# Kernel optimization log

Measured on AMD Instinct MI355X. Metric: run time of the kernel, lower is better.

Reference implementation:

```python
import jax, jax.numpy as jnp
import numpy as np

NUM_MID = 10   # hard-coded num_mid_nodes in HiPool.__init__
NUM_HIGH = 5   # ceil(10 / 2)


def map_low_to_high(num_low, num_high):
    # eye(num_high) repeat_interleaved by ceil(low/high) rows, truncated to num_low
    # == one-hot of i // edges_per_high
    edges_per_high = -(-num_low // num_high)
    return jax.nn.one_hot(jnp.arange(num_low) // edges_per_high, num_high,
                          dtype=jnp.float32)  # [low, high]


def cluster_attention(x, mapping, att):
    # x: [s, d], mapping: [s, m], att: [d, d]
    mid = mapping.T @ x                              # [m, d]
    scores = (mid @ att) @ x.T                       # [m, s]
    scores = scores * (1.0 - mapping).T              # zero (not -inf) own-cluster entries, as in source
    scores = jax.nn.softmax(scores, axis=1)
    return scores @ x + mid                          # [m, d]


def dense_gcn(x, adj, W, b):
    # torch_geometric DenseGCNConv with add_loop=True
    n = adj.shape[0]
    i = jnp.arange(n)
    adj = adj.at[i, i].set(1.0)
    deg = jnp.clip(jnp.sum(adj, axis=-1), 1.0, None) ** -0.5
    adj = deg[:, None] * adj * deg[None, :]
    return adj @ (x @ W) + b


def setup_inputs() -> dict:
    key = jax.random.key(0)
    ks = jax.random.split(key, 8)
    S, D, H = 8192, 768, 768
    return {
        "x": jax.random.normal(ks[0], (S, D), dtype=jnp.float32),
        "adjacency_matrix": jax.random.uniform(ks[1], (S, S), dtype=jnp.float32),
        "att_low_mid": jax.random.normal(ks[2], (D, D), dtype=jnp.float32) * 0.04,  # xavier_normal-ish
        "conv1_w": jax.random.normal(ks[3], (D, H), dtype=jnp.float32) * 0.04,
        "conv1_b": jnp.zeros((H,), dtype=jnp.float32),
        "att_mid_high": jax.random.normal(ks[4], (H, H), dtype=jnp.float32) * 0.04,
        "conv2_w": jax.random.normal(ks[5], (H, H), dtype=jnp.float32) * 0.04,
        "conv2_b": jnp.zeros((H,), dtype=jnp.float32),
    }


def reference(x, adjacency_matrix, att_low_mid, conv1_w, conv1_b,
              att_mid_high, conv2_w, conv2_b):
    s = x.shape[0]
    m1 = map_low_to_high(s, NUM_MID)                         # [s, 10]
    mid_adj = m1.T @ adjacency_matrix @ m1                   # [10, 10]
    mid_rep = cluster_attention(x, m1, att_low_mid)          # [10, d]
    x_mid = jax.nn.relu(dense_gcn(mid_rep, mid_adj, conv1_w, conv1_b))
    # F.dropout(...)[0]: dropout treated as identity (eval); [0] just dropped the batch dim
    m2 = map_low_to_high(NUM_MID, NUM_HIGH)                  # [10, 5]
    high_adj = m2.T @ mid_adj @ m2                           # [5, 5]
    high_rep = cluster_attention(x_mid, m2, att_mid_high)    # [5, h]
    out = jax.nn.relu(dense_gcn(high_rep, high_adj, conv2_w, conv2_b))
    return out.mean(axis=0)                                  # [h]
```

## Files before the change

### kernel.cpp

```cpp
#include <hip/hip_runtime.h>

constexpr int S    = 8192;
constexpr int D    = 768;
constexpr int NMID = 10;
constexpr int EPH  = 820;
constexpr int TAILB = 48;

constexpr int PART_ADJ = 0;
constexpr int PART_MID = 3200;
constexpr int OFF_Y1   = 64640;
constexpr int OFF_Z2   = 72320;
constexpr int OFF_MATT = 76160;
constexpr int OFF_XMID = 83840;
constexpr int OFF_MID2 = 91520;
constexpr int OFF_SCB  = 95360;
constexpr int OFF_PVP  = 97920;
constexpr int OFF_BAR  = 1081344;

__device__ __forceinline__ void adj_partial(const float* __restrict__ A,
                                            float* __restrict__ ws, int item) {
    __shared__ float wred[4];
    int p = item >> 5, s = item & 31;
    int i = p / 10, j = p % 10;
    int r0 = i * EPH, nr = min(EPH, S - r0);
    int c0 = j * EPH, nc = min(EPH, S - c0);
    int rs0 = r0 + (nr * s) / 32, rs1 = r0 + (nr * (s + 1)) / 32;
    int nc4 = nc >> 2;
    int tid = threadIdx.x;
    float acc = 0.f;
    for (int r = rs0; r < rs1; ++r) {
        const float4* row = (const float4*)(A + (size_t)r * S + c0);
        if (tid < nc4) {
            float4 v = row[tid];
            acc += (v.x + v.y) + (v.z + v.w);
        }
    }
#pragma unroll
    for (int off = 32; off > 0; off >>= 1) acc += __shfl_down(acc, off, 64);
    int ln = tid & 63, wv = tid >> 6;
    if (ln == 0) wred[wv] = acc;
    __syncthreads();
    if (tid == 0) ws[PART_ADJ + item] = (wred[0] + wred[1]) + (wred[2] + wred[3]);
}

__device__ __forceinline__ void mid_partial(const float* __restrict__ x,
                                            float* __restrict__ ws, int item) {
    int cl = item / 24, rem = item % 24;
    int cc = rem >> 3, sp = rem & 7;
    int r0 = cl * EPH, nr = min(EPH, S - r0);
    int rs0 = r0 + (nr * sp) / 8, rs1 = r0 + (nr * (sp + 1)) / 8;
    int c = cc * 256 + threadIdx.x;
    float acc = 0.f;
    for (int r = rs0; r < rs1; ++r) acc += x[(size_t)r * D + c];
    ws[PART_MID + (sp * NMID + cl) * D + c] = acc;
}

template <int NR>
__device__ __forceinline__ void mm_core(const float* __restrict__ W,
                                        const float* mi,
                                        float* __restrict__ out, int kb) {
    int c = threadIdx.x;
    float a0[NR], a1[NR], a2[NR];
#pragma unroll
    for (int i = 0; i < NR; ++i) { a0[i] = 0.f; a1[i] = 0.f; a2[i] = 0.f; }
    for (int kk = 0; kk < 16; ++kk) {
        const float* wr = W + (size_t)(kb + kk) * D;
        float w0 = wr[c], w1 = wr[c + 256], w2 = wr[c + 512];
#pragma unroll
        for (int i = 0; i < NR; ++i) {
            float m = mi[i * 16 + kk];
            a0[i] += m * w0; a1[i] += m * w1; a2[i] += m * w2;
        }
    }
#pragma unroll
    for (int i = 0; i < NR; ++i) {
        atomicAdd(&out[i * D + c],       a0[i]);
        atomicAdd(&out[i * D + c + 256], a1[i]);
        atomicAdd(&out[i * D + c + 512], a2[i]);
    }
}

template <int NR>
__device__ __forceinline__ void fullk_slice(const float* __restrict__ W,
                                            const float* inL, float* red,
                                            float* outS, int c0) {
    int tid = threadIdx.x;
    int c = tid & 15, ks = tid >> 4;
    float acc[NR];
#pragma unroll
    for (int i = 0; i < NR; ++i) acc[i] = 0.f;
    int kb = ks * 48;
    for (int kk = 0; kk < 48; ++kk) {
        int k = kb + kk;
        float w = W[(size_t)k * D + c0 + c];
#pragma unroll
        for (int i = 0; i < NR; ++i) acc[i] += inL[i * D + k] * w;
    }
#pragma unroll
    for (int i = 0; i < NR; ++i) red[(ks * NR + i) * 16 + c] = acc[i];
    __syncthreads();
    if (tid < NR * 16) {
        int i = tid >> 4, cc = tid & 15;
        float s = 0.f;
#pragma unroll
        for (int k2 = 0; k2 < 16; ++k2) s += red[(k2 * NR + i) * 16 + cc];
        outS[i * 16 + cc] = s;
    }
    __syncthreads();
}

__device__ __forceinline__ void gbar(unsigned* bar) {
    __syncthreads();
    if (threadIdx.x == 0) {
        __threadfence();
        unsigned g = __hip_atomic_load(bar + 32, __ATOMIC_RELAXED, __HIP_MEMORY_SCOPE_AGENT);
        unsigned a = __hip_atomic_fetch_add(bar, 1u, __ATOMIC_ACQ_REL, __HIP_MEMORY_SCOPE_AGENT);
        if (a == (unsigned)(TAILB - 1)) {
            __hip_atomic_store(bar, 0u, __ATOMIC_RELAXED, __HIP_MEMORY_SCOPE_AGENT);
            __hip_atomic_fetch_add(bar + 32, 1u, __ATOMIC_RELEASE, __HIP_MEMORY_SCOPE_AGENT);
        } else {
            while (__hip_atomic_load(bar + 32, __ATOMIC_ACQUIRE, __HIP_MEMORY_SCOPE_AGENT) == g)
                __builtin_amdgcn_s_sleep(8);
        }
        __threadfence();
    }
    __syncthreads();
}

__global__ __launch_bounds__(256) void k1(const float* __restrict__ A,
                                          const float* __restrict__ x,
                                          float* __restrict__ ws) {
    int bx = blockIdx.x, tid = threadIdx.x;
    if (bx < 1280) adj_partial(A, ws, bx);
    else if (bx < 1520) mid_partial(x, ws, bx - 1280);
    else {
        int b = bx - 1520;
        for (int t = b * 256 + tid; t < 11520; t += 768) ws[OFF_Y1 + t] = 0.f;
        if (b == 0 && tid < 64) ((unsigned*)(ws + OFF_BAR))[tid] = 0u;
    }
}

__global__ __launch_bounds__(256) void k2(const float* __restrict__ attL,
                                          const float* __restrict__ A,
                                          float* __restrict__ ws) {
    int bx = blockIdx.x, tid = threadIdx.x;
    if (bx >= 48) { adj_partial(A, ws, 1280 + bx - 48); return; }
    __shared__ float midL[7680];
    __shared__ float red[2560];
    __shared__ float outS[160];
    for (int t = tid; t < 7680; t += 256) {
        int cl = t / D, k = t - cl * D;
        float s = 0.f;
#pragma unroll
        for (int sp = 0; sp < 8; ++sp)
            s += ws[PART_MID + (sp * NMID + cl) * D + k];
        midL[t] = s;
    }
    __syncthreads();
    fullk_slice<10>(attL, midL, red, outS, bx * 16);
    if (tid < 160) ws[OFF_MATT + (tid >> 4) * D + bx * 16 + (tid & 15)] = outS[tid];
}

__global__ __launch_bounds__(256) void k3(const float* __restrict__ x,
                                          const float* __restrict__ A,
                                          float* __restrict__ ws) {
    int bx = blockIdx.x, tid = threadIdx.x;
    if (bx >= 128) { adj_partial(A, ws, 2240 + bx - 128); return; }
    __shared__ float ma[7680];
    __shared__ float sl[640];
    __shared__ float mloc[10];
    for (int t = tid; t < 7680; t += 256) ma[t] = ws[OFF_MATT + t];
    __syncthreads();
    const float4* maf = (const float4*)ma;
    const float4* x4  = (const float4*)x;
    int wave = tid >> 6, ln = tid & 63;
    int r0 = bx * 64;
    for (int rr = 0; rr < 16; ++rr) {
        int rl = wave * 16 + rr;
        int r = r0 + rl;
        float4 v0 = x4[(size_t)r * 192 + ln];
        float4 v1 = x4[(size_t)r * 192 + 64 + ln];
        float4 v2 = x4[(size_t)r * 192 + 128 + ln];
        int rc = r / EPH;
#pragma unroll
        for (int i = 0; i < NMID; ++i) {
            float4 m0 = maf[i * 192 + ln];
            float4 m1 = maf[i * 192 + 64 + ln];
            float4 m2 = maf[i * 192 + 128 + ln];
            float p = m0.x * v0.x + m0.y * v0.y + m0.z * v0.z + m0.w * v0.w
                    + m1.x * v1.x + m1.y * v1.y + m1.z * v1.z + m1.w * v1.w
                    + m2.x * v2.x + m2.y * v2.y + m2.z * v2.z + m2.w * v2.w;
#pragma unroll
            for (int off = 32; off > 0; off >>= 1) p += __shfl_down(p, off, 64);
            if (ln == 0) sl[rl * NMID + i] = (rc == i) ? 0.f : p;
        }
    }
    __syncthreads();
    if (tid < NMID) {
        float m = -1e30f;
        for (int r = 0; r < 64; ++r) m = fmaxf(m, sl[r * NMID + tid]);
        float s = 0.f;
        for (int r = 0; r < 64; ++r) s += expf(sl[r * NMID + tid] - m);
        mloc[tid] = m;
        ws[OFF_SCB + bx * 20 + tid * 2]     = m;
        ws[OFF_SCB + bx * 20 + tid * 2 + 1] = s;
    }
    __syncthreads();
    for (int t = tid; t < 640; t += 256) sl[t] = expf(sl[t] - mloc[t % NMID]);
    __syncthreads();
    float a0[NMID], a1[NMID], a2[NMID];
#pragma unroll
    for (int i = 0; i < NMID; ++i) { a0[i] = 0.f; a1[i] = 0.f; a2[i] = 0.f; }
    for (int r = 0; r < 64; ++r) {
        const float* xr = x + (size_t)(r0 + r) * D;
        float x0 = xr[tid], x1 = xr[tid + 256], x2 = xr[tid + 512];
#pragma unroll
        for (int i = 0; i < NMID; ++i) {
            float w = sl[r * NMID + i];
            a0[i] += w * x0; a1[i] += w * x1; a2[i] += w * x2;
        }
    }
#pragma unroll
    for (int i = 0; i < NMID; ++i) {
        float* base = ws + OFF_PVP + (bx * NMID + i) * D;
        base[tid]       = a0[i];
        base[tid + 256] = a1[i];
        base[tid + 512] = a2[i];
    }
}

__global__ __launch_bounds__(256) void k4(const float* __restrict__ W1,
                                          const float* __restrict__ b1,
                                          const float* __restrict__ attH,
                                          const float* __restrict__ W2,
                                          const float* __restrict__ b2,
                                          float* __restrict__ ws,
                                          float* __restrict__ out) {
    __shared__ float lm[160], ls[160], Mi[16], Zi[16];
    __shared__ float wts[1280];
    __shared__ float mi[160];
    __shared__ float aa[100], dg[16], NM[100], xml[160], mi2[80];
    __shared__ float sred[200], s2l[64], P2[50];
    __shared__ float out2L[3840], red[1280], Y2s[80];
    __shared__ float ha[32], dh[8], NH[32];
    unsigned* bar = (unsigned*)(ws + OFF_BAR);
    int bx = blockIdx.x, tid = threadIdx.x;
    int kb = bx * 16;

    if (tid < 160) {
        int i = tid >> 4, seg = tid & 15;
        float m = -1e30f;
        for (int b = seg * 8; b < seg * 8 + 8; ++b)
            m = fmaxf(m, ws[OFF_SCB + b * 20 + i * 2]);
        float s = 0.f;
        for (int b = seg * 8; b < seg * 8 + 8; ++b)
            s += ws[OFF_SCB + b * 20 + i * 2 + 1] *
                 expf(ws[OFF_SCB + b * 20 + i * 2] - m);
        lm[tid] = m; ls[tid] = s;
    }
    __syncthreads();
    if (tid < NMID) {
        float M = -1e30f;
        for (int g = 0; g < 16; ++g) M = fmaxf(M, lm[tid * 16 + g]);
        float Z = 0.f;
        for (int g = 0; g < 16; ++g) Z += ls[tid * 16 + g] * expf(lm[tid * 16 + g] - M);
        Mi[tid] = M; Zi[tid] = 1.f / Z;
    }
    __syncthreads();
    for (int t = tid; t < 1280; t += 256) {
        int b = t / NMID, i = t % NMID;
        wts[t] = expf(ws[OFF_SCB + b * 20 + i * 2] - Mi[i]) * Zi[i];
    }
    __syncthreads();
    if (tid < 160) {
        int i = tid >> 4, k = kb + (tid & 15);
        float s = 0.f;
#pragma unroll
        for (int sp = 0; sp < 8; ++sp)
            s += ws[PART_MID + (sp * NMID + i) * D + k];
        for (int b = 0; b < 128; ++b)
            s += wts[b * NMID + i] * ws[OFF_PVP + (b * NMID + i) * D + k];
        mi[tid] = s;
    }
    __syncthreads();
    mm_core<10>(W1, mi, ws + OFF_Y1, kb);

    gbar(bar);

    if (tid < 100) {
        float s = 0.f;
#pragma unroll
        for (int sp = 0; sp < 32; ++sp) s += ws[PART_ADJ + tid * 32 + sp];
        aa[tid] = s;
    }
    __syncthreads();
    if (tid < 10) {
        float s = 0.f;
#pragma unroll
        for (int j = 0; j < 10; ++j) s += (tid == j) ? 1.f : aa[tid * 10 + j];
        dg[tid] = 1.f / sqrtf(fmaxf(s, 1.f));
    }
    __syncthreads();
    if (tid < 100) {
        int i = tid / 10, j = tid % 10;
        NM[tid] = dg[i] * ((i == j) ? 1.f : aa[tid]) * dg[j];
    }
    __syncthreads();
    if (tid < 160) {
        int i = tid >> 4, c = kb + (tid & 15);
        float v = b1[c];
#pragma unroll
        for (int j = 0; j < 10; ++j) v += NM[i * 10 + j] * ws[OFF_Y1 + j * D + c];
        float xm = fmaxf(v, 0.f);
        ws[OFF_XMID + i * D + c] = xm;
        xml[tid] = xm;
    }
    __syncthreads();
    if (tid < 80) {
        int a = tid >> 4, cc = tid & 15;
        float m2v = xml[(2 * a) * 16 + cc] + xml[(2 * a + 1) * 16 + cc];
        ws[OFF_MID2 + a * D + kb + cc] = m2v;
        mi2[tid] = m2v;
    }
    __syncthreads();
    mm_core<5>(attH, mi2, ws + OFF_Z2, kb);

    gbar(bar);

    if (tid < 200) {
        int pp = tid >> 2, q = tid & 3;
        int i = pp / 10, r = pp % 10;
        const float* z  = ws + OFF_Z2 + i * D;
        const float* xm = ws + OFF_XMID + r * D;
        float s = 0.f;
        for (int c = q * 192; c < q * 192 + 192; ++c) s += z[c] * xm[c];
        sred[tid] = s;
    }
    __syncthreads();
    if (tid < 50) {
        int i = tid / 10, r = tid % 10;
        float v = sred[tid * 4] + sred[tid * 4 + 1] + sred[tid * 4 + 2] + sred[tid * 4 + 3];
        s2l[tid] = ((r >> 1) == i) ? 0.f : v;
    }
    __syncthreads();
    if (tid < 5) {
        float mx = -1e30f;
#pragma unroll
        for (int r = 0; r < 10; ++r) mx = fmaxf(mx, s2l[tid * 10 + r]);
        float sm = 0.f; float e[10];
#pragma unroll
        for (int r = 0; r < 10; ++r) { e[r] = expf(s2l[tid * 10 + r] - mx); sm += e[r]; }
#pragma unroll
        for (int r = 0; r < 10; ++r) P2[tid * 10 + r] = e[r] / sm;
    }
    __syncthreads();
    for (int t = tid; t < 3840; t += 256) {
        int i = t / D, k = t - i * D;
        float v = ws[OFF_MID2 + t];
#pragma unroll
        for (int r = 0; r < 10; ++r) v += P2[i * 10 + r] * ws[OFF_XMID + r * D + k];
        out2L[t] = v;
    }
    __syncthreads();
    fullk_slice<5>(W2, out2L, red, Y2s, kb);
    if (tid < 25) {
        int a = tid / 5, b = tid % 5;
        ha[tid] = aa[(2 * a) * 10 + 2 * b] + aa[(2 * a) * 10 + 2 * b + 1]
                + aa[(2 * a + 1) * 10 + 2 * b] + aa[(2 * a + 1) * 10 + 2 * b + 1];
    }
    __syncthreads();
    if (tid < 5) {
        float s = 0.f;
#pragma unroll
        for (int j = 0; j < 5; ++j) s += (tid == j) ? 1.f : ha[tid * 5 + j];
        dh[tid] = 1.f / sqrtf(fmaxf(s, 1.f));
    }
    __syncthreads();
    if (tid < 25) {
        int i = tid / 5, j = tid % 5;
        NH[tid] = dh[i] * ((i == j) ? 1.f : ha[tid]) * dh[j];
    }
    __syncthreads();
    if (tid < 16) {
        int c = kb + tid;
        float bias = b2[c];
        float s = 0.f;
#pragma unroll
        for (int i = 0; i < 5; ++i) {
            float v = bias;
#pragma unroll
            for (int j = 0; j < 5; ++j) v += NH[i * 5 + j] * Y2s[j * 16 + tid];
            s += fmaxf(v, 0.f);
        }
        out[c] = s * 0.2f;
    }
}

extern "C" void kernel_launch(void* const* d_in, const int* in_sizes, int n_in,
                              void* d_out, int out_size, void* d_ws, size_t ws_size,
                              hipStream_t stream) {
    const float* x    = (const float*)d_in[0];
    const float* adj  = (const float*)d_in[1];
    const float* attL = (const float*)d_in[2];
    const float* W1   = (const float*)d_in[3];
    const float* b1   = (const float*)d_in[4];
    const float* attH = (const float*)d_in[5];
    const float* W2   = (const float*)d_in[6];
    const float* b2   = (const float*)d_in[7];
    float* ws  = (float*)d_ws;
    float* out = (float*)d_out;

    k1<<<1523, 256, 0, stream>>>(adj, x, ws);
    k2<<<1008, 256, 0, stream>>>(attL, adj, ws);
    k3<<<1088, 256, 0, stream>>>(x, adj, ws);
    k4<<<TAILB, 256, 0, stream>>>(W1, b1, attH, W2, b2, ws, out);
}
```

Measured before the change: 177.8 us.

## Replace adjacency block-tiling with full-row bucketed sums and split tail kernel

Adjacency cluster sums are now computed per full row strip: each block reads whole rows with 8 float4 loads per thread and buckets the sums into 10 column clusters in shared memory. This replaces 32-way splitting of each of the 100 tiles and gives 400 work items instead of 3200, so there are far fewer blocks in the overlapped kernels. The grid-barrier tail kernel is split into two launches (k4 computing Y1, then k5). In k5 every block redundantly recomputes the GCN output, mid2 and the full attH projection into shared memory instead of synchronising through global memory. This removes the spin barriers, but each of the 48 blocks now does the full 768x768x5 product.

Measured after the change: 270.4 us. +52.1%, slower.

```diff
diff --git a/kernel.cpp b/kernel.cpp
--- a/kernel.cpp
+++ b/kernel.cpp
@@ -4,43 +4,58 @@
 constexpr int D    = 768;
 constexpr int NMID = 10;
 constexpr int EPH  = 820;
-constexpr int TAILB = 48;
+
+constexpr int ADJ_SPLIT = 40;
+constexpr int N_ADJ = 10 * ADJ_SPLIT;
 
 constexpr int PART_ADJ = 0;
-constexpr int PART_MID = 3200;
-constexpr int OFF_Y1   = 64640;
-constexpr int OFF_Z2   = 72320;
-constexpr int OFF_MATT = 76160;
-constexpr int OFF_XMID = 83840;
-constexpr int OFF_MID2 = 91520;
-constexpr int OFF_SCB  = 95360;
-constexpr int OFF_PVP  = 97920;
-constexpr int OFF_BAR  = 1081344;
-
-__device__ __forceinline__ void adj_partial(const float* __restrict__ A,
-                                            float* __restrict__ ws, int item) {
-    __shared__ float wred[4];
-    int p = item >> 5, s = item & 31;
-    int i = p / 10, j = p % 10;
+constexpr int PART_MID = 4096;
+constexpr int OFF_Y1   = 65536;
+constexpr int OFF_MATT = 73216;
+constexpr int OFF_SCB  = 80896;
+constexpr int OFF_PVP  = 83456;
+
+__device__ __forceinline__ void adj_item(const float* __restrict__ A,
+                                         float* __restrict__ ws, int item) {
+    __shared__ float bucket[2560];
+    __shared__ float red2[160];
+    int i = item / ADJ_SPLIT, s = item % ADJ_SPLIT;
     int r0 = i * EPH, nr = min(EPH, S - r0);
-    int c0 = j * EPH, nc = min(EPH, S - c0);
-    int rs0 = r0 + (nr * s) / 32, rs1 = r0 + (nr * (s + 1)) / 32;
-    int nc4 = nc >> 2;
+    int rs0 = r0 + nr * s / ADJ_SPLIT, rs1 = r0 + nr * (s + 1) / ADJ_SPLIT;
     int tid = threadIdx.x;
-    float acc = 0.f;
+    float acc[8];
+#pragma unroll
+    for (int u = 0; u < 8; ++u) acc[u] = 0.f;
     for (int r = rs0; r < rs1; ++r) {
-        const float4* row = (const float4*)(A + (size_t)r * S + c0);
-        if (tid < nc4) {
-            float4 v = row[tid];
-            acc += (v.x + v.y) + (v.z + v.w);
-        }
-    }
-#pragma unroll
-    for (int off = 32; off > 0; off >>= 1) acc += __shfl_down(acc, off, 64);
-    int ln = tid & 63, wv = tid >> 6;
-    if (ln == 0) wred[wv] = acc;
-    __syncthreads();
-    if (tid == 0) ws[PART_ADJ + item] = (wred[0] + wred[1]) + (wred[2] + wred[3]);
+        const float4* row = (const float4*)(A + (size_t)r * S);
+#pragma unroll
+        for (int u = 0; u < 8; ++u) {
+            float4 v = row[tid + 256 * u];
+            acc[u] += (v.x + v.y) + (v.z + v.w);
+        }
+    }
+    for (int t = tid; t < 2560; t += 256) bucket[t] = 0.f;
+    __syncthreads();
+#pragma unroll
+    for (int u = 0; u < 8; ++u) {
+        int j = ((tid + 256 * u) * 4) / 820;
+        bucket[j * 256 + tid] += acc[u];
+    }
+    __syncthreads();
+    if (tid < 160) {
+        int j = tid >> 4, seg = tid & 15;
+        float sm = 0.f;
+#pragma unroll
+        for (int u = 0; u < 16; ++u) sm += bucket[j * 256 + seg * 16 + u];
+        red2[tid] = sm;
+    }
+    __syncthreads();
+    if (tid < 10) {
+        float sm = 0.f;
+#pragma unroll
+        for (int g = 0; g < 16; ++g) sm += red2[tid * 16 + g];
+        ws[PART_ADJ + item * 10 + tid] = sm;
+    }
 }
 
 __device__ __forceinline__ void mid_partial(const float* __restrict__ x,
@@ -109,34 +124,16 @@
     __syncthreads();
 }
 
-__device__ __forceinline__ void gbar(unsigned* bar) {
-    __syncthreads();
-    if (threadIdx.x == 0) {
-        __threadfence();
-        unsigned g = __hip_atomic_load(bar + 32, __ATOMIC_RELAXED, __HIP_MEMORY_SCOPE_AGENT);
-        unsigned a = __hip_atomic_fetch_add(bar, 1u, __ATOMIC_ACQ_REL, __HIP_MEMORY_SCOPE_AGENT);
-        if (a == (unsigned)(TAILB - 1)) {
-            __hip_atomic_store(bar, 0u, __ATOMIC_RELAXED, __HIP_MEMORY_SCOPE_AGENT);
-            __hip_atomic_fetch_add(bar + 32, 1u, __ATOMIC_RELEASE, __HIP_MEMORY_SCOPE_AGENT);
-        } else {
-            while (__hip_atomic_load(bar + 32, __ATOMIC_ACQUIRE, __HIP_MEMORY_SCOPE_AGENT) == g)
-                __builtin_amdgcn_s_sleep(8);
-        }
-        __threadfence();
-    }
-    __syncthreads();
-}
-
 __global__ __launch_bounds__(256) void k1(const float* __restrict__ A,
                                           const float* __restrict__ x,
                                           float* __restrict__ ws) {
-    int bx = blockIdx.x, tid = threadIdx.x;
-    if (bx < 1280) adj_partial(A, ws, bx);
-    else if (bx < 1520) mid_partial(x, ws, bx - 1280);
+    int bx = blockIdx.x;
+    if (bx < 240) mid_partial(x, ws, bx);
+    else if (bx < 500) adj_item(A, ws, bx - 240);
     else {
-        int b = bx - 1520;
-        for (int t = b * 256 + tid; t < 11520; t += 768) ws[OFF_Y1 + t] = 0.f;
-        if (b == 0 && tid < 64) ((unsigned*)(ws + OFF_BAR))[tid] = 0u;
+        int b = bx - 500;
+        for (int t = b * 256 + threadIdx.x; t < 7680; t += 512)
+            ws[OFF_Y1 + t] = 0.f;
     }
 }
 
@@ -144,7 +141,7 @@
                                           const float* __restrict__ A,
                                           float* __restrict__ ws) {
     int bx = blockIdx.x, tid = threadIdx.x;
-    if (bx >= 48) { adj_partial(A, ws, 1280 + bx - 48); return; }
+    if (bx >= 48) { adj_item(A, ws, 260 + bx - 48); return; }
     __shared__ float midL[7680];
     __shared__ float red[2560];
     __shared__ float outS[160];
@@ -165,7 +162,7 @@
                                           const float* __restrict__ A,
                                           float* __restrict__ ws) {
     int bx = blockIdx.x, tid = threadIdx.x;
-    if (bx >= 128) { adj_partial(A, ws, 2240 + bx - 128); return; }
+    if (bx >= 128) { adj_item(A, ws, 330 + bx - 128); return; }
     __shared__ float ma[7680];
     __shared__ float sl[640];
     __shared__ float mloc[10];
@@ -230,23 +227,11 @@
 }
 
 __global__ __launch_bounds__(256) void k4(const float* __restrict__ W1,
-                                          const float* __restrict__ b1,
-                                          const float* __restrict__ attH,
-                                          const float* __restrict__ W2,
-                                          const float* __restrict__ b2,
-                                          float* __restrict__ ws,
-                                          float* __restrict__ out) {
+                                          float* __restrict__ ws) {
     __shared__ float lm[160], ls[160], Mi[16], Zi[16];
     __shared__ float wts[1280];
     __shared__ float mi[160];
-    __shared__ float aa[100], dg[16], NM[100], xml[160], mi2[80];
-    __shared__ float sred[200], s2l[64], P2[50];
-    __shared__ float out2L[3840], red[1280], Y2s[80];
-    __shared__ float ha[32], dh[8], NH[32];
-    unsigned* bar = (unsigned*)(ws + OFF_BAR);
-    int bx = blockIdx.x, tid = threadIdx.x;
-    int kb = bx * 16;
-
+    int tid = threadIdx.x, kb = blockIdx.x * 16;
     if (tid < 160) {
         int i = tid >> 4, seg = tid & 15;
         float m = -1e30f;
@@ -284,13 +269,30 @@
     }
     __syncthreads();
     mm_core<10>(W1, mi, ws + OFF_Y1, kb);
-
-    gbar(bar);
+}
+
+__global__ __launch_bounds__(256) void k5(const float* __restrict__ attH,
+                                          const float* __restrict__ b1,
+                                          const float* __restrict__ W2,
+                                          const float* __restrict__ b2,
+                                          float* __restrict__ ws,
+                                          float* __restrict__ out) {
+    __shared__ float xmidL[7680];
+    __shared__ float mid2L[3840];
+    __shared__ float z2L[3840];
+    __shared__ float out2L[3840];
+    __shared__ float red[1280];
+    __shared__ float Y2s[80];
+    __shared__ float aa[100], dg[16], NM[100];
+    __shared__ float sred[200], s2l[64], P2[50];
+    __shared__ float ha[32], dh[8], NH[32];
+    int tid = threadIdx.x, kb = blockIdx.x * 16;
 
     if (tid < 100) {
-        float s = 0.f;
-#pragma unroll
-        for (int sp = 0; sp < 32; ++sp) s += ws[PART_ADJ + tid * 32 + sp];
+        int i = tid / 10, j = tid % 10;
+        float s = 0.f;
+        for (int sp = 0; sp < ADJ_SPLIT; ++sp)
+            s += ws[PART_ADJ + (i * ADJ_SPLIT + sp) * 10 + j];
         aa[tid] = s;
     }
     __syncthreads();
@@ -306,34 +308,45 @@
         NM[tid] = dg[i] * ((i == j) ? 1.f : aa[tid]) * dg[j];
     }
     __syncthreads();
-    if (tid < 160) {
-        int i = tid >> 4, c = kb + (tid & 15);
-        float v = b1[c];
-#pragma unroll
-        for (int j = 0; j < 10; ++j) v += NM[i * 10 + j] * ws[OFF_Y1 + j * D + c];
-        float xm = fmaxf(v, 0.f);
-        ws[OFF_XMID + i * D + c] = xm;
-        xml[tid] = xm;
-    }
-    __syncthreads();
-    if (tid < 80) {
-        int a = tid >> 4, cc = tid & 15;
-        float m2v = xml[(2 * a) * 16 + cc] + xml[(2 * a + 1) * 16 + cc];
-        ws[OFF_MID2 + a * D + kb + cc] = m2v;
-        mi2[tid] = m2v;
-    }
-    __syncthreads();
-    mm_core<5>(attH, mi2, ws + OFF_Z2, kb);
-
-    gbar(bar);
-
+    for (int c = tid; c < D; c += 256) {
+        float yv[10];
+#pragma unroll
+        for (int j = 0; j < 10; ++j) yv[j] = ws[OFF_Y1 + j * D + c];
+        float bias = b1[c];
+        float xm[10];
+#pragma unroll
+        for (int i = 0; i < 10; ++i) {
+            float v = bias;
+#pragma unroll
+            for (int j = 0; j < 10; ++j) v += NM[i * 10 + j] * yv[j];
+            xm[i] = fmaxf(v, 0.f);
+            xmidL[i * D + c] = xm[i];
+        }
+#pragma unroll
+        for (int a = 0; a < 5; ++a)
+            mid2L[a * D + c] = xm[2 * a] + xm[2 * a + 1];
+    }
+    __syncthreads();
+    for (int q = 0; q < 3; ++q) {
+        int c = q * 256 + tid;
+        float accz[5];
+#pragma unroll
+        for (int a = 0; a < 5; ++a) accz[a] = 0.f;
+        for (int k = 0; k < D; ++k) {
+            float w = attH[(size_t)k * D + c];
+#pragma unroll
+            for (int a = 0; a < 5; ++a) accz[a] += mid2L[a * D + k] * w;
+        }
+#pragma unroll
+        for (int a = 0; a < 5; ++a) z2L[a * D + c] = accz[a];
+    }
+    __syncthreads();
     if (tid < 200) {
         int pp = tid >> 2, q = tid & 3;
         int i = pp / 10, r = pp % 10;
-        const float* z  = ws + OFF_Z2 + i * D;
-        const float* xm = ws + OFF_XMID + r * D;
-        float s = 0.f;
-        for (int c = q * 192; c < q * 192 + 192; ++c) s += z[c] * xm[c];
+        float s = 0.f;
+        for (int c = q * 192; c < q * 192 + 192; ++c)
+            s += z2L[i * D + c] * xmidL[r * D + c];
         sred[tid] = s;
     }
     __syncthreads();
@@ -356,9 +369,9 @@
     __syncthreads();
     for (int t = tid; t < 3840; t += 256) {
         int i = t / D, k = t - i * D;
-        float v = ws[OFF_MID2 + t];
-#pragma unroll
-        for (int r = 0; r < 10; ++r) v += P2[i * 10 + r] * ws[OFF_XMID + r * D + k];
+        float v = mid2L[t];
+#pragma unroll
+        for (int r = 0; r < 10; ++r) v += P2[i * 10 + r] * xmidL[r * D + k];
         out2L[t] = v;
     }
     __syncthreads();
@@ -410,8 +423,9 @@
     float* ws  = (float*)d_ws;
     float* out = (float*)d_out;
 
-    k1<<<1523, 256, 0, stream>>>(adj, x, ws);
-    k2<<<1008, 256, 0, stream>>>(attL, adj, ws);
-    k3<<<1088, 256, 0, stream>>>(x, adj, ws);
-    k4<<<TAILB, 256, 0, stream>>>(W1, b1, attH, W2, b2, ws, out);
-}
+    k1<<<502, 256, 0, stream>>>(adj, x, ws);
+    k2<<<118, 256, 0, stream>>>(attL, adj, ws);
+    k3<<<198, 256, 0, stream>>>(x, adj, ws);
+    k4<<<48,  256, 0, stream>>>(W1, ws);
+    k5<<<48,  256, 0, stream>>>(attH, b1, W2, b2, ws, out);
+}
```
